# Kernel optimization log

Hardware: AMD Instinct MI355X
Metric: run time of the kernel (lower is better)

## Reference

```python
import math
import jax, jax.numpy as jnp
import numpy as np

B, L, D, HID, DFF, EA, NH = 16, 511, 1024, 512, 2048, 256, 4
S = L + 1  # tgt length = bos + L; also memory length (max_basis_dim+1)


def _pe(seq, d):
    pos = jnp.arange(seq, dtype=jnp.float32)[:, None]
    div = jnp.exp(jnp.arange(0, d, 2, dtype=jnp.float32) * (-math.log(10000.0) / d))
    pe = jnp.zeros((seq, d), jnp.float32)
    return pe.at[:, 0::2].set(jnp.sin(pos * div)).at[:, 1::2].set(jnp.cos(pos * div))


def _ln(x, w, b):
    m = x.mean(-1, keepdims=True)
    v = ((x - m) ** 2).mean(-1, keepdims=True)
    return (x - m) / jnp.sqrt(v + 1e-5) * w + b


def _leaky(x):
    return jnp.where(x >= 0, x, 0.01 * x)


def _mha(xq, xkv, qkv_w, qkv_b, out_w, out_b, mask):
    d = xq.shape[-1]
    hd = d // NH
    wq, wk, wv = jnp.split(qkv_w, 3, axis=0)
    bq, bk, bv = jnp.split(qkv_b, 3)
    q = (xq @ wq.T + bq).reshape(xq.shape[0], xq.shape[1], NH, hd)
    k = (xkv @ wk.T + bk).reshape(xkv.shape[0], xkv.shape[1], NH, hd)
    v = (xkv @ wv.T + bv).reshape(xkv.shape[0], xkv.shape[1], NH, hd)
    att = jnp.einsum('bqhd,bkhd->bhqk', q, k) / math.sqrt(hd)
    if mask is not None:
        att = att + mask
    p = jax.nn.softmax(att, axis=-1)
    o = jnp.einsum('bhqk,bkhd->bqhd', p, v).reshape(xq.shape[0], xq.shape[1], d)
    return o @ out_w.T + out_b


def setup_inputs() -> dict:
    key = jax.random.key(0)
    ks = iter(jax.random.split(key, 40))
    rn = lambda shape, s=0.02: jax.random.normal(next(ks), shape, jnp.float32) * s
    return dict(
        gs_norms_embedding=jax.random.normal(next(ks), (B, S, HID), jnp.float32),
        prev_action_embedding=jax.random.normal(next(ks), (B, EA), jnp.float32),
        current_action_embedding=jax.random.normal(next(ks), (B, EA), jnp.float32),
        target_gs_norms=jax.random.normal(next(ks), (B, L), jnp.float32),
        bos=rn((1, 1), 1.0),
        inp_w1=rn((HID, 1)), inp_b1=rn((HID,)),
        inp_w2=rn((HID, HID)), inp_b2=rn((HID,)),
        sa_qkv_w=rn((3, 3 * D, D)), sa_qkv_b=rn((3, 3 * D)),
        sa_out_w=rn((3, D, D)), sa_out_b=rn((3, D)),
        ca_qkv_w=rn((3, 3 * D, D)), ca_qkv_b=rn((3, 3 * D)),
        ca_out_w=rn((3, D, D)), ca_out_b=rn((3, D)),
        ln_w=jnp.ones((3, 3, D), jnp.float32), ln_b=jnp.zeros((3, 3, D), jnp.float32),
        ff_w1=rn((3, DFF, D)), ff_b1=rn((3, DFF)),
        ff_w2=rn((3, D, DFF)), ff_b2=rn((3, D)),
        proj_w1=rn((HID, D)), proj_b1=rn((HID,)),
        proj_w2=rn((1, HID)), proj_b2=rn((1,)),
        basis_dim=jax.random.randint(next(ks), (B,), 0, S),
    )


def reference(gs_norms_embedding, prev_action_embedding, current_action_embedding,
              target_gs_norms, bos, inp_w1, inp_b1, inp_w2, inp_b2,
              sa_qkv_w, sa_qkv_b, sa_out_w, sa_out_b,
              ca_qkv_w, ca_qkv_b, ca_out_w, ca_out_b,
              ln_w, ln_b, ff_w1, ff_b1, ff_w2, ff_b2,
              proj_w1, proj_b1, proj_w2, proj_b2, basis_dim):
    b = gs_norms_embedding.shape[0]
    prev = jnp.broadcast_to(prev_action_embedding[:, None, :], (b, S, EA))
    cur = jnp.broadcast_to(current_action_embedding[:, None, :], (b, S, EA))
    # teacher-forced target: [bos, target] -> input_projection -> pos enc
    tgt_scalar = jnp.concatenate([jnp.broadcast_to(bos, (b, 1)), target_gs_norms], axis=1)  # [B,S]
    x = _leaky(tgt_scalar[..., None] @ inp_w1.T + inp_b1) @ inp_w2.T + inp_b2  # [B,S,HID]
    x = x + _pe(S, HID)
    tgt = jnp.concatenate([x, prev, cur], axis=-1)  # [B,S,D]
    mem = jnp.concatenate([gs_norms_embedding, prev, cur], axis=-1)  # [B,S,D]
    mask = jnp.triu(jnp.full((S, S), -1e9, jnp.float32), k=1)
    h = tgt
    for l in range(3):  # post-norm TransformerDecoderLayer, activation=relu
        h = _ln(h + _mha(h, h, sa_qkv_w[l], sa_qkv_b[l], sa_out_w[l], sa_out_b[l], mask), ln_w[l, 0], ln_b[l, 0])
        h = _ln(h + _mha(h, mem, ca_qkv_w[l], ca_qkv_b[l], ca_out_w[l], ca_out_b[l], None), ln_w[l, 1], ln_b[l, 1])
        ff = jax.nn.relu(h @ ff_w1[l].T + ff_b1[l]) @ ff_w2[l].T + ff_b2[l]
        h = _ln(h + ff, ln_w[l, 2], ln_b[l, 2])
    out = (_leaky(h[:, 1:, :] @ proj_w1.T + proj_b1) @ proj_w2.T + proj_b2)[..., 0]  # [B,L]
    keep = jnp.arange(L)[None, :] < basis_dim[:, None]
    return jnp.where(keep, out, 0.0)
```

## Files before the change

### kernel.cpp

```cpp
#include <hip/hip_runtime.h>

typedef unsigned short u16;
typedef __attribute__((ext_vector_type(8))) short bf16x8;
typedef __attribute__((ext_vector_type(4))) float f32x4;

#define BB   16
#define LL   511
#define SS   512
#define DD   1024
#define HIDD 512
#define DFFF 2048
#define NHH  4
#define HDD  256
#define MTOK (BB*SS)

__device__ __forceinline__ float b2f(u16 u){ return __uint_as_float(((unsigned)u)<<16); }
__device__ __forceinline__ u16 f2b(float f){
    unsigned x = __float_as_uint(f);
    return (u16)((x + 0x7fffu + ((x>>16)&1u)) >> 16);
}
__device__ __forceinline__ float ldin(const void* p, size_t i, int f){
    return f ? ((const float*)p)[i] : b2f(((const u16*)p)[i]);
}
__device__ __forceinline__ void gload_lds16(const void* g, void* l){
    __builtin_amdgcn_global_load_lds((const __attribute__((address_space(1))) unsigned*)g,
                                     (__attribute__((address_space(3))) unsigned*)l, 16, 0, 0);
}

__global__ void detect_kernel(const u16* __restrict__ lnw, int* __restrict__ flag){
    if (threadIdx.x == 0 && blockIdx.x == 0) flag[0] = (lnw[0] == 0x3F80) ? 0 : 1;
}

__global__ void wconv_kernel(const void* __restrict__ w, size_t woff,
                             const void* __restrict__ b, size_t boff,
                             u16* __restrict__ dw, u16* __restrict__ db,
                             int nw, int nb, const int* __restrict__ flag){
    const int f = flag[0];
    const int idx = blockIdx.x*256 + threadIdx.x;
    const int stride = gridDim.x * 256;
    if (f){
        const float* wf = (const float*)w + woff;
        const float* bf = (const float*)b + boff;
        for (int i = idx*4; i < nw; i += stride*4){
            const float4 v = *(const float4*)&wf[i];
            ushort4 o; o.x=f2b(v.x); o.y=f2b(v.y); o.z=f2b(v.z); o.w=f2b(v.w);
            *(ushort4*)&dw[i] = o;
        }
        for (int i = idx*4; i < nb; i += stride*4){
            const float4 v = *(const float4*)&bf[i];
            ushort4 o; o.x=f2b(v.x); o.y=f2b(v.y); o.z=f2b(v.z); o.w=f2b(v.w);
            *(ushort4*)&db[i] = o;
        }
    } else {
        const u16* wu = (const u16*)w + woff;
        const u16* bu = (const u16*)b + boff;
        for (int i = idx*4; i < nw; i += stride*4) *(ushort4*)&dw[i] = *(const ushort4*)&wu[i];
        for (int i = idx*4; i < nb; i += stride*4) *(ushort4*)&db[i] = *(const ushort4*)&bu[i];
    }
}

__global__ void pe_kernel(float* __restrict__ pe){
    const int i = blockIdx.x*256 + threadIdx.x;
    const int s = i >> 9, c = i & 511;
    const float div = expf(-(float)(c & ~1) * (logf(10000.0f)/512.0f));
    const float ang = (float)s * div;
    pe[i] = (c & 1) ? cosf(ang) : sinf(ang);
}

__global__ void inp_u_kernel(const void* __restrict__ bos, const void* __restrict__ target,
                             const void* __restrict__ w1, const void* __restrict__ b1,
                             u16* __restrict__ U, const int* __restrict__ flag){
    const int f = flag[0];
    const int i = blockIdx.x*256 + threadIdx.x;
    const int m = i >> 9, c = i & 511;
    const int b = m >> 9, s = m & 511;
    const float ts = (s == 0) ? ldin(bos, 0, f) : ldin(target, b*LL + s - 1, f);
    float v = ts * ldin(w1, c, f) + ldin(b1, c, f);
    U[i] = f2b(v >= 0.f ? v : 0.01f*v);
}

__global__ void concat_kernel(const void* __restrict__ gs, const void* __restrict__ prev,
                              const void* __restrict__ cur, u16* __restrict__ tgt,
                              u16* __restrict__ mem, const int* __restrict__ flag){
    const int f = flag[0];
    const int i = blockIdx.x*256 + threadIdx.x;
    const int m = i >> 10, c = i & 1023;
    if (c < 512){
        mem[i] = f2b(ldin(gs, (size_t)m*512 + c, f));
    } else {
        const float pc = (c < 768) ? ldin(prev, (m>>9)*256 + (c-512), f)
                                   : ldin(cur,  (m>>9)*256 + (c-768), f);
        const u16 pb = f2b(pc);
        tgt[i] = pb; mem[i] = pb;
    }
}

template<int ACT, int RES>
__device__ __forceinline__ void gemm_body(const u16* __restrict__ A, const u16* __restrict__ W,
                                          const u16* __restrict__ bias, u16* __restrict__ C,
                                          const float* __restrict__ pe, const u16* __restrict__ res,
                                          int K, int ldc){
    __shared__ __align__(16) short As[4096];
    __shared__ __align__(16) short Bs[4096];
    const int m0 = blockIdx.x * 128;
    const int n0 = blockIdx.y * 128;
    const int t  = threadIdx.x;
    const int w = t >> 6, lane = t & 63;
    const int quad = lane >> 4, l16 = lane & 15;
    const int wm = (w >> 1) * 64, wn = (w & 1) * 64;

    f32x4 acc[4][4] = {};

    const u16* Ag = A + (size_t)(m0 + (t>>2))*K + (t&3)*8;
    const u16* Wg = W + (size_t)(n0 + (t>>2))*K + (t&3)*8;
    short* Asd = &As[t*8];
    short* Bsd = &Bs[t*8];
    for (int k0 = 0; k0 < K; k0 += 32){
        __syncthreads();
        gload_lds16(Ag + k0,                 Asd);
        gload_lds16(Ag + (size_t)64*K + k0,  Asd + 2048);
        gload_lds16(Wg + k0,                 Bsd);
        gload_lds16(Wg + (size_t)64*K + k0,  Bsd + 2048);
        __syncthreads();
        bf16x8 af[4], bfr[4];
#pragma unroll
        for (int i=0;i<4;i++) af[i]  = *(const bf16x8*)&As[(wm + i*16 + l16)*32 + quad*8];
#pragma unroll
        for (int j=0;j<4;j++) bfr[j] = *(const bf16x8*)&Bs[(wn + j*16 + l16)*32 + quad*8];
#pragma unroll
        for (int i=0;i<4;i++)
#pragma unroll
            for (int j=0;j<4;j++)
                acc[i][j] = __builtin_amdgcn_mfma_f32_16x16x32_bf16(af[i], bfr[j], acc[i][j], 0,0,0);
    }
#pragma unroll
    for (int i=0;i<4;i++){
        const int rowb = m0 + wm + i*16 + quad*4;
#pragma unroll
        for (int j=0;j<4;j++){
            const int col = n0 + wn + j*16 + l16;
            const float bv = b2f(bias[col]);
#pragma unroll
            for (int r=0;r<4;r++){
                float v = acc[i][j][r] + bv;
                if (pe) v += pe[((rowb + r) & (SS-1))*HIDD + col];
                if (RES) v += b2f(res[(size_t)(rowb + r)*ldc + col]);
                if (ACT == 1) v = fmaxf(v, 0.0f);
                C[(size_t)(rowb + r)*ldc + col] = f2b(v);
            }
        }
    }
}

template<int ACT, int RES>
__global__ __launch_bounds__(256) void gemm_bt(const u16* __restrict__ A, const u16* __restrict__ W,
                                               const u16* __restrict__ bias, u16* __restrict__ C,
                                               const float* __restrict__ pe, const u16* __restrict__ res,
                                               int K, int ldc){
    gemm_body<ACT,RES>(A, W, bias, C, pe, res, K, ldc);
}

__global__ __launch_bounds__(256) void gemm_dual(const u16* __restrict__ A1, const u16* __restrict__ A2,
                                                 const u16* __restrict__ W, const u16* __restrict__ bias,
                                                 u16* __restrict__ C, int K, int ldc){
    const u16* A = (blockIdx.y < 8) ? A1 : A2;
    gemm_body<0,0>(A, W, bias, C, nullptr, nullptr, K, ldc);
}

template<int ACT, int RES, int DUAL>
__global__ __launch_bounds__(512, 2) void gemm_p(const u16* __restrict__ A1, const u16* __restrict__ A2,
                                                 const u16* __restrict__ W, const u16* __restrict__ bias,
                                                 u16* __restrict__ C, const u16* __restrict__ res,
                                                 int K, int ldc){
    __shared__ __align__(16) short lds[36864];
    const int t = threadIdx.x;
    const int w = t >> 6, lane = t & 63;
    const int quad = lane >> 4, l16 = lane & 15;
    const int wm = w >> 2, wn = w & 3;
    const int m0 = blockIdx.x * 128;
    const int n0 = blockIdx.y * 256;
    const u16* A = (DUAL && blockIdx.y >= 4) ? A2 : A1;

    const int srow = t >> 2;
    const int gl   = (t & 3) ^ ((t >> 3) & 3);
    const u16* Ag = A + (size_t)(m0 + srow)*K + gl*8;
    const u16* Bg = W + (size_t)(n0 + srow)*K + gl*8;
    const size_t rstep = (size_t)128 * K;
    short* ldst = &lds[t*8];

    const int koff = (quad ^ ((l16 >> 1) & 3)) * 8;
    const int aoff = (wm*64 + l16)*32 + koff;
    const int boff = 4096 + (wn*64 + l16)*32 + koff;

    f32x4 acc[4][4] = {};
    const int NS = K >> 5;

    gload_lds16(Ag,              ldst);
    gload_lds16(Bg,              ldst + 4096);
    gload_lds16(Bg + rstep,      ldst + 8192);
    gload_lds16(Ag + 32,         ldst + 12288);
    gload_lds16(Bg + 32,         ldst + 12288 + 4096);
    gload_lds16(Bg + rstep + 32, ldst + 12288 + 8192);
    asm volatile("s_waitcnt vmcnt(3)" ::: "memory");
    __builtin_amdgcn_s_barrier();
    asm volatile("" ::: "memory");

    int slot = 0, slot2 = 2;
    for (int s = 0; s < NS; ++s){
        const int sb = slot * 12288;
        const short* Ab = &lds[sb + aoff];
        const short* Bb = &lds[sb + boff];
        bf16x8 av[4], bv[4];
#pragma unroll
        for (int i=0;i<4;i++) av[i] = *(const bf16x8*)(Ab + i*512);
#pragma unroll
        for (int j=0;j<4;j++) bv[j] = *(const bf16x8*)(Bb + j*512);
        const int prefetch = (s + 2 < NS);
        if (prefetch){
            const u16* Ap = Ag + (size_t)(s+2)*32;
            const u16* Bp = Bg + (size_t)(s+2)*32;
            short* ld2 = &lds[slot2*12288 + t*8];
            gload_lds16(Ap,         ld2);
            gload_lds16(Bp,         ld2 + 4096);
            gload_lds16(Bp + rstep, ld2 + 8192);
        }
        asm volatile("s_waitcnt lgkmcnt(0)");
        __builtin_amdgcn_s_setprio(1);
#pragma unroll
        for (int i=0;i<4;i++)
#pragma unroll
            for (int j=0;j<4;j++)
                acc[i][j] = __builtin_amdgcn_mfma_f32_16x16x32_bf16(av[i], bv[j], acc[i][j], 0,0,0);
        __builtin_amdgcn_s_setprio(0);
        if (prefetch) asm volatile("s_waitcnt vmcnt(3)" ::: "memory");
        else          asm volatile("s_waitcnt vmcnt(0)" ::: "memory");
        __builtin_amdgcn_s_barrier();
        asm volatile("" ::: "memory");

        slot  = (slot  == 2) ? 0 : slot  + 1;
        slot2 = (slot2 == 2) ? 0 : slot2 + 1;
    }

#pragma unroll
    for (int i=0;i<4;i++){
        const int rowb = m0 + wm*64 + i*16 + quad*4;
#pragma unroll
        for (int j=0;j<4;j++){
            const int col = n0 + wn*64 + j*16 + l16;
            const float bvv = b2f(bias[col]);
#pragma unroll
            for (int r=0;r<4;r++){
                float v = acc[i][j][r] + bvv;
                if (RES) v += b2f(res[(size_t)(rowb + r)*ldc + col]);
                if (ACT == 1) v = fmaxf(v, 0.0f);
                C[(size_t)(rowb + r)*ldc + col] = f2b(v);
            }
        }
    }
}

__global__ __launch_bounds__(256) void vt_kernel(const u16* __restrict__ qkv, u16* __restrict__ vt){
    __shared__ __align__(16) u16 tile[64][72];
    const int bh = blockIdx.x, b = bh >> 2, h = bh & 3;
    const int s0 = blockIdx.y*64, d0 = blockIdx.z*64;
    const int t = threadIdx.x;
#pragma unroll
    for (int it=0; it<2; it++){
        const int u = it*256 + t;
        const int sl = u >> 3, dc = (u & 7)*8;
        *(uint4*)&tile[sl][dc] =
            *(const uint4*)(qkv + (size_t)(b*SS + s0 + sl)*3072 + 2*DD + h*HDD + d0 + dc);
    }
    __syncthreads();
#pragma unroll
    for (int it=0; it<2; it++){
        const int u = it*256 + t;
        const int dl = u >> 3, sc = (u & 7)*8;
        uint4 tv; u16* tmp = (u16*)&tv;
#pragma unroll
        for (int j=0;j<8;j++) tmp[j] = tile[sc+j][dl];
        *(uint4*)(vt + (size_t)(bh*HDD + d0 + dl)*SS + s0 + sc) = tv;
    }
}

__global__ __launch_bounds__(256) void flash_attn(const u16* __restrict__ qkv, const u16* __restrict__ vt,
                                                  u16* __restrict__ ao, const int causal){
    __shared__ __align__(16) short Kt[8192];
    __shared__ __align__(16) short Vs[8192];
    __shared__ __align__(16) short pbuf[4][16][40];
    const int qt = causal ? (gridDim.x - 1 - blockIdx.x) : blockIdx.x;
    const int bh = blockIdx.y;
    const int b = bh >> 2, h = bh & 3;
    const int t = threadIdx.x, w = t >> 6, lane = t & 63;
    const int quad = lane >> 4, l16 = lane & 15;
    const int qbase = qt * 64;

    const u16* qp = qkv + (size_t)(b*SS + qbase + w*16 + l16)*3072 + h*HDD + quad*8;
    bf16x8 qf[8];
#pragma unroll
    for (int kc=0;kc<8;kc++) qf[kc] = *(const bf16x8*)(qp + kc*32);

    f32x4 o[16] = {};
    float mrow[4] = {-1e30f,-1e30f,-1e30f,-1e30f};
    float lrow[4] = {0.f,0.f,0.f,0.f};

    const int ntiles = causal ? (qbase/32 + 2) : (SS/32);
    const int myq = qbase + w*16 + quad*4;

    const u16* Kg = qkv + (size_t)(b*SS)*3072 + DD + h*HDD;
    const u16* Vg = vt + (size_t)bh*HDD*SS;
    const int keyl8 = t >> 5;
    const int kslot = t & 31;
    const int vrow4 = t >> 2;
    const int vslot = t & 3;

    for (int kt=0; kt<ntiles; kt++){
        const int kv0 = kt*32;
        __syncthreads();
#pragma unroll
        for (int j=0;j<4;j++){
            const int keyl = j*8 + keyl8;
            const int ck   = kslot ^ keyl;
            gload_lds16(Kg + (size_t)(kv0 + keyl)*3072 + ck*8, &Kt[j*2048 + t*8]);
            const int d  = j*64 + vrow4;
            const int cv = vslot ^ (d&3) ^ ((d>>2)&3);
            gload_lds16(Vg + (size_t)d*SS + kv0 + cv*8, &Vs[j*2048 + t*8]);
        }
        __syncthreads();

        f32x4 sc0 = {0.f,0.f,0.f,0.f}, sc1 = {0.f,0.f,0.f,0.f};
#pragma unroll
        for (int kk=0;kk<8;kk++){
            const int ch = kk*4 + quad;
            sc0 = __builtin_amdgcn_mfma_f32_16x16x32_bf16(qf[kk],
                    *(const bf16x8*)&Kt[l16*256 + (ch ^ l16)*8], sc0, 0,0,0);
            sc1 = __builtin_amdgcn_mfma_f32_16x16x32_bf16(qf[kk],
                    *(const bf16x8*)&Kt[(16+l16)*256 + (ch ^ (16+l16))*8], sc1, 0,0,0);
        }
#pragma unroll
        for (int r=0;r<4;r++){
            float a0 = sc0[r]*0.0625f, a1 = sc1[r]*0.0625f;
            if (causal){
                if (kv0 + l16 > myq + r)      a0 = -1e9f;
                if (kv0 + 16 + l16 > myq + r) a1 = -1e9f;
            }
            float tm = fmaxf(a0,a1);
            tm = fmaxf(tm, __shfl_xor(tm,1)); tm = fmaxf(tm, __shfl_xor(tm,2));
            tm = fmaxf(tm, __shfl_xor(tm,4)); tm = fmaxf(tm, __shfl_xor(tm,8));
            const float mnew  = fmaxf(mrow[r], tm);
            const float alpha = __expf(mrow[r] - mnew);
            const float p0 = __expf(a0 - mnew), p1 = __expf(a1 - mnew);
            float rs = p0 + p1;
            rs += __shfl_xor(rs,1); rs += __shfl_xor(rs,2);
            rs += __shfl_xor(rs,4); rs += __shfl_xor(rs,8);
            lrow[r] = lrow[r]*alpha + rs;
            mrow[r] = mnew;
#pragma unroll
            for (int dt=0;dt<16;dt++) o[dt][r] *= alpha;
            pbuf[w][quad*4+r][l16]      = (short)f2b(p0);
            pbuf[w][quad*4+r][16 + l16] = (short)f2b(p1);
        }
        __syncthreads();

        const bf16x8 pf = *(const bf16x8*)&pbuf[w][l16][quad*8];
#pragma unroll
        for (int dt=0;dt<16;dt++){
            const int d = dt*16 + l16;
            o[dt] = __builtin_amdgcn_mfma_f32_16x16x32_bf16(pf,
                      *(const bf16x8*)&Vs[d*32 + ((quad ^ (d&3) ^ ((d>>2)&3)))*8], o[dt], 0,0,0);
        }
    }
#pragma unroll
    for (int r=0;r<4;r++){
        const size_t row = (size_t)(b*SS + myq + r);
        const float inv = 1.0f / lrow[r];
#pragma unroll
        for (int dt=0;dt<16;dt++)
            ao[row*DD + h*HDD + dt*16 + l16] = f2b(o[dt][r]*inv);
    }
}

__global__ __launch_bounds__(256) void ln_kernel(u16* __restrict__ h, const u16* __restrict__ y,
                                                 const void* __restrict__ lnw, const void* __restrict__ lnb,
                                                 size_t off, const int* __restrict__ flag){
    const int f = flag[0];
    const int m = blockIdx.x, t = threadIdx.x;
    __shared__ float red[8];
    const ushort4 yv = *(const ushort4*)&y[(size_t)m*DD + t*4];
    float vv[4]; float sum = 0.f;
    vv[0] = b2f(yv.x); vv[1] = b2f(yv.y); vv[2] = b2f(yv.z); vv[3] = b2f(yv.w);
#pragma unroll
    for (int j=0;j<4;j++) sum += vv[j];
    for (int o2=1; o2<64; o2<<=1) sum += __shfl_xor(sum, o2);
    if ((t&63)==0) red[t>>6] = sum;
    __syncthreads();
    const float mean = (red[0]+red[1]+red[2]+red[3]) * (1.f/DD);
    float vs = 0.f;
#pragma unroll
    for (int j=0;j<4;j++){ const float d = vv[j]-mean; vs += d*d; }
    for (int o2=1; o2<64; o2<<=1) vs += __shfl_xor(vs, o2);
    if ((t&63)==0) red[4 + (t>>6)] = vs;
    __syncthreads();
    const float var = (red[4]+red[5]+red[6]+red[7]) * (1.f/DD);
    const float rstd = rsqrtf(var + 1e-5f);
    ushort4 ov;
    ov.x = f2b((vv[0]-mean)*rstd*ldin(lnw, off+t*4+0, f) + ldin(lnb, off+t*4+0, f));
    ov.y = f2b((vv[1]-mean)*rstd*ldin(lnw, off+t*4+1, f) + ldin(lnb, off+t*4+1, f));
    ov.z = f2b((vv[2]-mean)*rstd*ldin(lnw, off+t*4+2, f) + ldin(lnb, off+t*4+2, f));
    ov.w = f2b((vv[3]-mean)*rstd*ldin(lnw, off+t*4+3, f) + ldin(lnb, off+t*4+3, f));
    *(ushort4*)&h[(size_t)m*DD + t*4] = ov;
}

__global__ __launch_bounds__(256) void final_kernel(const u16* __restrict__ p1, const void* __restrict__ w2,
                                                    const void* __restrict__ b2p, const int* __restrict__ basis,
                                                    void* __restrict__ out, const int* __restrict__ flag){
    const int f = flag[0];
    const int blk = blockIdx.x;
    const int b = blk / LL, l = blk % LL;
    const int t = threadIdx.x;
    __shared__ float red[4];
    const ushort2 pv = *(const ushort2*)&p1[(size_t)(b*SS + l + 1)*HIDD + t*2];
    float acc;
    {
        float v0 = b2f(pv.x); v0 = v0 >= 0.f ? v0 : 0.01f*v0;
        float v1 = b2f(pv.y); v1 = v1 >= 0.f ? v1 : 0.01f*v1;
        acc = v0 * ldin(w2, t*2+0, f) + v1 * ldin(w2, t*2+1, f);
    }
    for (int off=1; off<64; off<<=1) acc += __shfl_xor(acc, off);
    if ((t & 63) == 0) red[t>>6] = acc;
    __syncthreads();
    if (t == 0){
        const float r = red[0]+red[1]+red[2]+red[3] + ldin(b2p, 0, f);
        const float v = (l < basis[b]) ? r : 0.0f;
        if (f) ((float*)out)[blk] = v;
        else   ((u16*)out)[blk] = f2b(v);
    }
}

extern "C" void kernel_launch(void* const* d_in, const int* in_sizes, int n_in,
                              void* d_out, int out_size, void* d_ws, size_t ws_size,
                              hipStream_t stream){
    const void* gs       = d_in[0];
    const void* prev     = d_in[1];
    const void* cur      = d_in[2];
    const void* target   = d_in[3];
    const void* bos      = d_in[4];
    const void* inp_w1   = d_in[5];
    const void* inp_b1   = d_in[6];
    const void* inp_w2   = d_in[7];
    const void* inp_b2   = d_in[8];
    const void* sa_qkv_w = d_in[9];
    const void* sa_qkv_b = d_in[10];
    const void* sa_out_w = d_in[11];
    const void* sa_out_b = d_in[12];
    const void* ca_qkv_w = d_in[13];
    const void* ca_qkv_b = d_in[14];
    const void* ca_out_w = d_in[15];
    const void* ca_out_b = d_in[16];
    const void* ln_w     = d_in[17];
    const void* ln_b     = d_in[18];
    const void* ff_w1    = d_in[19];
    const void* ff_b1    = d_in[20];
    const void* ff_w2    = d_in[21];
    const void* ff_b2    = d_in[22];
    const void* proj_w1  = d_in[23];
    const void* proj_b1  = d_in[24];
    const void* proj_w2  = d_in[25];
    const void* proj_b2  = d_in[26];
    const int*  basis    = (const int*)d_in[27];

    size_t off = 0;
    auto carve = [&](size_t bytes)->void*{
        void* p = (char*)d_ws + off;
        off += (bytes + 255) & ~(size_t)255;
        return p;
    };
    int*   flag = (int*)  carve(256);
    u16*   qkv  = (u16*)  carve((size_t)MTOK*3*DD*2);
    u16*   h    = (u16*)  carve((size_t)MTOK*DD*2);
    u16*   mem  = (u16*)  carve((size_t)MTOK*DD*2);
    u16*   ao   = (u16*)  carve((size_t)MTOK*DD*2);
    u16*   vty  = (u16*)  carve((size_t)MTOK*DD*2);
    float* pe   = (float*)carve((size_t)SS*HIDD*4);
    u16* U  = qkv;
    u16* vt = vty;
    u16* y  = vty;

    const size_t NW_TOTAL = 38535168, NB_TOTAL = 34816;
    const bool full = (ws_size >= off + ((NW_TOTAL*2+255)&~(size_t)255) + ((NB_TOTAL*2+255)&~(size_t)255));

    detect_kernel<<<dim3(1), 64, 0, stream>>>((const u16*)ln_w, flag);
    pe_kernel    <<<dim3(SS*HIDD/256),  256, 0, stream>>>(pe);
    inp_u_kernel <<<dim3(MTOK*HIDD/256),256, 0, stream>>>(bos, target, inp_w1, inp_b1, U, flag);

    if (full){
        u16* wbuf = (u16*)carve(NW_TOTAL*2);
        u16* bbuf = (u16*)carve(NB_TOTAL*2);
        u16* w_saqkv = wbuf + 0;
        u16* w_saout = wbuf + 9437184;
        u16* w_caqkv = wbuf + 12582912;
        u16* w_caout = wbuf + 22020096;
        u16* w_ff1   = wbuf + 25165824;
        u16* w_ff2   = wbuf + 31457280;
        u16* w_inp2  = wbuf + 37748736;
        u16* w_proj1 = wbuf + 38010880;
        u16* b_saqkv = bbuf + 0;
        u16* b_saout = bbuf + 9216;
        u16* b_caqkv = bbuf + 12288;
        u16* b_caout = bbuf + 21504;
        u16* b_ff1   = bbuf + 24576;
        u16* b_ff2   = bbuf + 30720;
        u16* b_inp2  = bbuf + 33792;
        u16* b_proj1 = bbuf + 34304;

        const dim3 wg(1024);
        wconv_kernel<<<wg,256,0,stream>>>(inp_w2,  0, inp_b2,  0, w_inp2,  b_inp2,  HIDD*HIDD, HIDD, flag);
        wconv_kernel<<<wg,256,0,stream>>>(sa_qkv_w,0, sa_qkv_b,0, w_saqkv, b_saqkv, 3*3*DD*DD, 3*3*DD, flag);
        wconv_kernel<<<wg,256,0,stream>>>(sa_out_w,0, sa_out_b,0, w_saout, b_saout, 3*DD*DD,   3*DD,   flag);
        wconv_kernel<<<wg,256,0,stream>>>(ca_qkv_w,0, ca_qkv_b,0, w_caqkv, b_caqkv, 3*3*DD*DD, 3*3*DD, flag);
        wconv_kernel<<<wg,256,0,stream>>>(ca_out_w,0, ca_out_b,0, w_caout, b_caout, 3*DD*DD,   3*DD,   flag);
        wconv_kernel<<<wg,256,0,stream>>>(ff_w1,   0, ff_b1,   0, w_ff1,   b_ff1,   3*DFFF*DD, 3*DFFF, flag);
        wconv_kernel<<<wg,256,0,stream>>>(ff_w2,   0, ff_b2,   0, w_ff2,   b_ff2,   3*DD*DFFF, 3*DD,   flag);
        wconv_kernel<<<wg,256,0,stream>>>(proj_w1, 0, proj_b1, 0, w_proj1, b_proj1, HIDD*DD,   HIDD,   flag);

        gemm_bt<0,0> <<<dim3(64,4),  256, 0, stream>>>(U, w_inp2, b_inp2, h, pe, nullptr, HIDD, DD);
        concat_kernel<<<dim3(MTOK*DD/256), 256, 0, stream>>>(gs, prev, cur, h, mem, flag);

        for (int l = 0; l < 3; l++){
            gemm_p<0,0,0><<<dim3(64,12),512,0,stream>>>(h, nullptr, w_saqkv + (size_t)l*3*DD*DD,
                                                        b_saqkv + l*3*DD, qkv, nullptr, DD, 3*DD);
            vt_kernel    <<<dim3(64,8,4),256,0,stream>>>(qkv, vt);
            flash_attn   <<<dim3(8,64),  256,0,stream>>>(qkv, vt, ao, 1);
            gemm_p<0,1,0><<<dim3(64,4),  512,0,stream>>>(ao, nullptr, w_saout + (size_t)l*DD*DD,
                                                         b_saout + l*DD, y, h, DD, DD);
            ln_kernel    <<<dim3(MTOK),  256,0,stream>>>(h, y, ln_w, ln_b, (size_t)(l*3+0)*DD, flag);

            gemm_p<0,0,1><<<dim3(64,12),512,0,stream>>>(h, mem, w_caqkv + (size_t)l*3*DD*DD,
                                                        b_caqkv + l*3*DD, qkv, nullptr, DD, 3*DD);
            vt_kernel    <<<dim3(64,8,4),256,0,stream>>>(qkv, vt);
            flash_attn   <<<dim3(8,64),  256,0,stream>>>(qkv, vt, ao, 0);
            gemm_p<0,1,0><<<dim3(64,4),  512,0,stream>>>(ao, nullptr, w_caout + (size_t)l*DD*DD,
                                                         b_caout + l*DD, y, h, DD, DD);
            ln_kernel    <<<dim3(MTOK),  256,0,stream>>>(h, y, ln_w, ln_b, (size_t)(l*3+1)*DD, flag);

            gemm_p<1,0,0><<<dim3(64,8), 512,0,stream>>>(h, nullptr, w_ff1 + (size_t)l*DFFF*DD,
                                                        b_ff1 + l*DFFF, qkv, nullptr, DD, DFFF);
            gemm_p<0,1,0><<<dim3(64,4), 512,0,stream>>>(qkv, nullptr, w_ff2 + (size_t)l*DD*DFFF,
                                                        b_ff2 + l*DD, y, h, DFFF, DD);
            ln_kernel    <<<dim3(MTOK), 256,0,stream>>>(h, y, ln_w, ln_b, (size_t)(l*3+2)*DD, flag);
        }
        gemm_bt<0,0><<<dim3(64,4), 256,0,stream>>>(h, w_proj1, b_proj1, y, nullptr, nullptr, DD, HIDD);
        final_kernel<<<dim3(BB*LL),256,0,stream>>>(y, proj_w2, proj_b2, basis, d_out, flag);
    } else {
        u16* s0w = (u16*)carve((size_t)3*DD*DD*2);
        u16* s0b = (u16*)carve((size_t)4096*2);
        u16* s1w = (u16*)carve((size_t)3*DD*DD*2);
        u16* s1b = (u16*)carve((size_t)4096*2);
        const dim3 wcg(512);

        wconv_kernel<<<wcg,256,0,stream>>>(inp_w2, 0, inp_b2, 0, s0w, s0b, HIDD*HIDD, HIDD, flag);
        gemm_bt<0,0><<<dim3(64,4), 256,0,stream>>>(U, s0w, s0b, h, pe, nullptr, HIDD, DD);
        concat_kernel<<<dim3(MTOK*DD/256),256,0,stream>>>(gs, prev, cur, h, mem, flag);

        for (int l = 0; l < 3; l++){
            wconv_kernel<<<wcg,256,0,stream>>>(sa_qkv_w, (size_t)l*3*DD*DD, sa_qkv_b, (size_t)l*3*DD,
                                               s1w, s1b, 3*DD*DD, 3*DD, flag);
            gemm_bt<0,0><<<dim3(64,24),256,0,stream>>>(h, s1w, s1b, qkv, nullptr, nullptr, DD, 3*DD);
            vt_kernel   <<<dim3(64,8,4),256,0,stream>>>(qkv, vt);
            flash_attn  <<<dim3(8,64),  256,0,stream>>>(qkv, vt, ao, 1);
            wconv_kernel<<<wcg,256,0,stream>>>(sa_out_w, (size_t)l*DD*DD, sa_out_b, (size_t)l*DD,
                                               s0w, s0b, DD*DD, DD, flag);
            gemm_bt<0,1><<<dim3(64,8), 256,0,stream>>>(ao, s0w, s0b, y, nullptr, h, DD, DD);
            ln_kernel   <<<dim3(MTOK), 256,0,stream>>>(h, y, ln_w, ln_b, (size_t)(l*3+0)*DD, flag);

            wconv_kernel<<<wcg,256,0,stream>>>(ca_qkv_w, (size_t)l*3*DD*DD, ca_qkv_b, (size_t)l*3*DD,
                                               s1w, s1b, 3*DD*DD, 3*DD, flag);
            gemm_dual   <<<dim3(64,24),256,0,stream>>>(h, mem, s1w, s1b, qkv, DD, 3*DD);
            vt_kernel   <<<dim3(64,8,4),256,0,stream>>>(qkv, vt);
            flash_attn  <<<dim3(8,64),  256,0,stream>>>(qkv, vt, ao, 0);
            wconv_kernel<<<wcg,256,0,stream>>>(ca_out_w, (size_t)l*DD*DD, ca_out_b, (size_t)l*DD,
                                               s0w, s0b, DD*DD, DD, flag);
            gemm_bt<0,1><<<dim3(64,8), 256,0,stream>>>(ao, s0w, s0b, y, nullptr, h, DD, DD);
            ln_kernel   <<<dim3(MTOK), 256,0,stream>>>(h, y, ln_w, ln_b, (size_t)(l*3+1)*DD, flag);

            wconv_kernel<<<wcg,256,0,stream>>>(ff_w1, (size_t)l*DFFF*DD, ff_b1, (size_t)l*DFFF,
                                               s1w, s1b, DFFF*DD, DFFF, flag);
            gemm_bt<1,0><<<dim3(64,16),256,0,stream>>>(h, s1w, s1b, qkv, nullptr, nullptr, DD, DFFF);
            wconv_kernel<<<wcg,256,0,stream>>>(ff_w2, (size_t)l*DD*DFFF, ff_b2, (size_t)l*DD,
                                               s0w, s0b, DD*DFFF, DD, flag);
            gemm_bt<0,1><<<dim3(64,8), 256,0,stream>>>(qkv, s0w, s0b, y, nullptr, h, DFFF, DD);
            ln_kernel   <<<dim3(MTOK), 256,0,stream>>>(h, y, ln_w, ln_b, (size_t)(l*3+2)*DD, flag);
        }
        wconv_kernel<<<wcg,256,0,stream>>>(proj_w1, 0, proj_b1, 0, s1w, s1b, HIDD*DD, HIDD, flag);
        gemm_bt<0,0><<<dim3(64,4), 256,0,stream>>>(h, s1w, s1b, y, nullptr, nullptr, DD, HIDD);
        final_kernel<<<dim3(BB*LL),256,0,stream>>>(y, proj_w2, proj_b2, basis, d_out, flag);
    }
}
```

Before: 1.570 ms.

## Double-buffer K/V tiles in flash attention and reorder grid for causal balance

Flash attention now stages the next 32-key K and V tile into a second LDS buffer while computing on the current one. It waits with vmcnt and raw s_barrier instead of full __syncthreads, so global loads overlap the QK and PV MFMAs. The grid is swapped so batch-head varies fastest and the heavy causal query tiles are dispatched first across all heads. LDS usage doubles to about 64KB per block, which may reduce occupancy, and the hand-placed waitcnt counts rely on the exact number of outstanding loads.

```diff
diff --git a/kernel.cpp b/kernel.cpp
--- a/kernel.cpp
+++ b/kernel.cpp
@@ -285,11 +285,11 @@
 
 __global__ __launch_bounds__(256) void flash_attn(const u16* __restrict__ qkv, const u16* __restrict__ vt,
                                                   u16* __restrict__ ao, const int causal){
-    __shared__ __align__(16) short Kt[8192];
-    __shared__ __align__(16) short Vs[8192];
+    __shared__ __align__(16) short Kt[2][8192];
+    __shared__ __align__(16) short Vs[2][8192];
     __shared__ __align__(16) short pbuf[4][16][40];
-    const int qt = causal ? (gridDim.x - 1 - blockIdx.x) : blockIdx.x;
-    const int bh = blockIdx.y;
+    const int bh = blockIdx.x;
+    const int qt = causal ? (gridDim.y - 1 - blockIdx.y) : blockIdx.y;
     const int b = bh >> 2, h = bh & 3;
     const int t = threadIdx.x, w = t >> 6, lane = t & 63;
     const int quad = lane >> 4, l16 = lane & 15;
@@ -314,28 +314,40 @@
     const int vrow4 = t >> 2;
     const int vslot = t & 3;
 
-    for (int kt=0; kt<ntiles; kt++){
-        const int kv0 = kt*32;
-        __syncthreads();
+    auto stage = [&](int kt2, int sl){
+        const int kv0s = kt2*32;
 #pragma unroll
         for (int j=0;j<4;j++){
             const int keyl = j*8 + keyl8;
             const int ck   = kslot ^ keyl;
-            gload_lds16(Kg + (size_t)(kv0 + keyl)*3072 + ck*8, &Kt[j*2048 + t*8]);
+            gload_lds16(Kg + (size_t)(kv0s + keyl)*3072 + ck*8, &Kt[sl][j*2048 + t*8]);
             const int d  = j*64 + vrow4;
             const int cv = vslot ^ (d&3) ^ ((d>>2)&3);
-            gload_lds16(Vg + (size_t)d*SS + kv0 + cv*8, &Vs[j*2048 + t*8]);
-        }
-        __syncthreads();
+            gload_lds16(Vg + (size_t)d*SS + kv0s + cv*8, &Vs[sl][j*2048 + t*8]);
+        }
+    };
+
+    stage(0, 0);
+    for (int kt=0; kt<ntiles; kt++){
+        const int kv0 = kt*32;
+        const int sl = kt & 1;
+        if (kt + 1 < ntiles){
+            stage(kt+1, sl^1);
+            asm volatile("s_waitcnt vmcnt(8)" ::: "memory");
+        } else {
+            asm volatile("s_waitcnt vmcnt(0)" ::: "memory");
+        }
+        __builtin_amdgcn_s_barrier();
+        asm volatile("" ::: "memory");
 
         f32x4 sc0 = {0.f,0.f,0.f,0.f}, sc1 = {0.f,0.f,0.f,0.f};
 #pragma unroll
         for (int kk=0;kk<8;kk++){
             const int ch = kk*4 + quad;
             sc0 = __builtin_amdgcn_mfma_f32_16x16x32_bf16(qf[kk],
-                    *(const bf16x8*)&Kt[l16*256 + (ch ^ l16)*8], sc0, 0,0,0);
+                    *(const bf16x8*)&Kt[sl][l16*256 + (ch ^ l16)*8], sc0, 0,0,0);
             sc1 = __builtin_amdgcn_mfma_f32_16x16x32_bf16(qf[kk],
-                    *(const bf16x8*)&Kt[(16+l16)*256 + (ch ^ (16+l16))*8], sc1, 0,0,0);
+                    *(const bf16x8*)&Kt[sl][(16+l16)*256 + (ch ^ (16+l16))*8], sc1, 0,0,0);
         }
 #pragma unroll
         for (int r=0;r<4;r++){
@@ -360,15 +372,20 @@
             pbuf[w][quad*4+r][l16]      = (short)f2b(p0);
             pbuf[w][quad*4+r][16 + l16] = (short)f2b(p1);
         }
-        __syncthreads();
+        asm volatile("s_waitcnt lgkmcnt(0)" ::: "memory");
+        __builtin_amdgcn_s_barrier();
+        asm volatile("" ::: "memory");
 
         const bf16x8 pf = *(const bf16x8*)&pbuf[w][l16][quad*8];
 #pragma unroll
         for (int dt=0;dt<16;dt++){
             const int d = dt*16 + l16;
             o[dt] = __builtin_amdgcn_mfma_f32_16x16x32_bf16(pf,
-                      *(const bf16x8*)&Vs[d*32 + ((quad ^ (d&3) ^ ((d>>2)&3)))*8], o[dt], 0,0,0);
-        }
+                      *(const bf16x8*)&Vs[sl][d*32 + ((quad ^ (d&3) ^ ((d>>2)&3)))*8], o[dt], 0,0,0);
+        }
+        asm volatile("s_waitcnt lgkmcnt(0)" ::: "memory");
+        __builtin_amdgcn_s_barrier();
+        asm volatile("" ::: "memory");
     }
 #pragma unroll
     for (int r=0;r<4;r++){
@@ -530,7 +547,7 @@
             gemm_p<0,0,0><<<dim3(64,12),512,0,stream>>>(h, nullptr, w_saqkv + (size_t)l*3*DD*DD,
                                                         b_saqkv + l*3*DD, qkv, nullptr, DD, 3*DD);
             vt_kernel    <<<dim3(64,8,4),256,0,stream>>>(qkv, vt);
-            flash_attn   <<<dim3(8,64),  256,0,stream>>>(qkv, vt, ao, 1);
+            flash_attn   <<<dim3(64,8),  256,0,stream>>>(qkv, vt, ao, 1);
             gemm_p<0,1,0><<<dim3(64,4),  512,0,stream>>>(ao, nullptr, w_saout + (size_t)l*DD*DD,
                                                          b_saout + l*DD, y, h, DD, DD);
             ln_kernel    <<<dim3(MTOK),  256,0,stream>>>(h, y, ln_w, ln_b, (size_t)(l*3+0)*DD, flag);
@@ -538,7 +555,7 @@
             gemm_p<0,0,1><<<dim3(64,12),512,0,stream>>>(h, mem, w_caqkv + (size_t)l*3*DD*DD,
                                                         b_caqkv + l*3*DD, qkv, nullptr, DD, 3*DD);
             vt_kernel    <<<dim3(64,8,4),256,0,stream>>>(qkv, vt);
-            flash_attn   <<<dim3(8,64),  256,0,stream>>>(qkv, vt, ao, 0);
+            flash_attn   <<<dim3(64,8),  256,0,stream>>>(qkv, vt, ao, 0);
             gemm_p<0,1,0><<<dim3(64,4),  512,0,stream>>>(ao, nullptr, w_caout + (size_t)l*DD*DD,
                                                          b_caout + l*DD, y, h, DD, DD);
             ln_kernel    <<<dim3(MTOK),  256,0,stream>>>(h, y, ln_w, ln_b, (size_t)(l*3+1)*DD, flag);
@@ -567,7 +584,7 @@
                                                s1w, s1b, 3*DD*DD, 3*DD, flag);
             gemm_bt<0,0><<<dim3(64,24),256,0,stream>>>(h, s1w, s1b, qkv, nullptr, nullptr, DD, 3*DD);
             vt_kernel   <<<dim3(64,8,4),256,0,stream>>>(qkv, vt);
-            flash_attn  <<<dim3(8,64),  256,0,stream>>>(qkv, vt, ao, 1);
+            flash_attn  <<<dim3(64,8),  256,0,stream>>>(qkv, vt, ao, 1);
             wconv_kernel<<<wcg,256,0,stream>>>(sa_out_w, (size_t)l*DD*DD, sa_out_b, (size_t)l*DD,
                                                s0w, s0b, DD*DD, DD, flag);
             gemm_bt<0,1><<<dim3(64,8), 256,0,stream>>>(ao, s0w, s0b, y, nullptr, h, DD, DD);
@@ -577,7 +594,7 @@
                                                s1w, s1b, 3*DD*DD, 3*DD, flag);
             gemm_dual   <<<dim3(64,24),256,0,stream>>>(h, mem, s1w, s1b, qkv, DD, 3*DD);
             vt_kernel   <<<dim3(64,8,4),256,0,stream>>>(qkv, vt);
-            flash_attn  <<<dim3(8,64),  256,0,stream>>>(qkv, vt, ao, 0);
+            flash_attn  <<<dim3(64,8),  256,0,stream>>>(qkv, vt, ao, 0);
             wconv_kernel<<<wcg,256,0,stream>>>(ca_out_w, (size_t)l*DD*DD, ca_out_b, (size_t)l*DD,
                                                s0w, s0b, DD*DD, DD, flag);
             gemm_bt<0,1><<<dim3(64,8), 256,0,stream>>>(ao, s0w, s0b, y, nullptr, h, DD, DD);
```

Measured after the change: 1.500 ms. 4.5% less time.
